# Optimization experiments

Measured on AMD Instinct MI355X. Metric: run time of the kernel, lower is better.

## Reference

```python
import jax, jax.numpy as jnp
import numpy as np

B, N, C, H = 8, 1024, 1024, 16
HD = C // H
SCALE = HD ** -0.5

def setup_inputs() -> dict:
    key = jax.random.key(0)
    k1, k2, k3, k4 = jax.random.split(key, 4)
    x = jax.random.normal(k1, (B, N, C), dtype=jnp.float32)
    # torch nn.Linear weights: [out, in]
    w_qkv = jax.random.normal(k2, (3 * C, C), dtype=jnp.float32) * (C ** -0.5)
    w_proj = jax.random.normal(k3, (C, C), dtype=jnp.float32) * (C ** -0.5)
    b_proj = jax.random.normal(k4, (C,), dtype=jnp.float32) * 0.02
    return {"x": x, "w_qkv": w_qkv, "w_proj": w_proj, "b_proj": b_proj}

def reference(x, w_qkv, w_proj, b_proj):
    Bv, Nv, Cv = x.shape
    # qkv projection (no bias); torch Linear: x @ W^T
    qkv = jnp.einsum('bnc,dc->bnd', x, w_qkv)
    qkv = qkv.reshape(Bv, Nv, 3, H, HD).transpose(2, 0, 3, 1, 4)  # [3,B,H,N,hd]
    q, k, v = qkv[0], qkv[1], qkv[2]
    attn = jnp.einsum('bhnd,bhmd->bhnm', q, k) * SCALE  # [B,H,N,N]
    attn = jax.nn.softmax(attn, axis=-1)
    out = jnp.einsum('bhnm,bhmd->bhnd', attn, v)
    out = out.transpose(0, 2, 1, 3).reshape(Bv, Nv, Cv)
    out = jnp.einsum('bnc,dc->bnd', out, w_proj) + b_proj
    return out
```

## Files before the change

kernel.cpp:

```cpp
#include <hip/hip_runtime.h>


typedef __attribute__((ext_vector_type(8))) short bf16x8;
typedef __attribute__((ext_vector_type(4))) short bf16x4;
typedef __attribute__((ext_vector_type(4))) float f32x4;

__device__ __forceinline__ short f2bf(float f) {
    union { float f; unsigned u; } x;
    x.f = f;
    unsigned r = x.u + 0x7fffu + ((x.u >> 16) & 1u);
    return (short)(r >> 16);
}

__device__ __forceinline__ void load_lds16(const void* g, void* l) {
    __builtin_amdgcn_global_load_lds((const __attribute__((address_space(1))) unsigned*)g,
                                     (__attribute__((address_space(3))) unsigned*)l,
                                     16, 0, 0);
}

__global__ __launch_bounds__(256) void convert_all(const float* __restrict__ x,
                                                   const float* __restrict__ wqkv,
                                                   const float* __restrict__ wproj,
                                                   short* __restrict__ xb,
                                                   short* __restrict__ wqkvb,
                                                   short* __restrict__ wprojb) {
    int i = blockIdx.x * 256 + threadIdx.x;
    const float* src;
    short* dst;
    int j;
    if (i < 2097152)      { src = x;     dst = xb;     j = i; }
    else if (i < 2883584) { src = wqkv;  dst = wqkvb;  j = i - 2097152; }
    else                  { src = wproj; dst = wprojb; j = i - 2883584; }
    float4 v = *(const float4*)(src + j * 4);
    unsigned lo = (unsigned short)f2bf(v.x) | ((unsigned)(unsigned short)f2bf(v.y) << 16);
    unsigned hi = (unsigned short)f2bf(v.z) | ((unsigned)(unsigned short)f2bf(v.w) << 16);
    uint2 p; p.x = lo; p.y = hi;
    *(uint2*)(dst + j * 4) = p;
}

template<int EPI, int BM, int BN, int NTX>
__global__ __launch_bounds__(512, 2) void gemm2p(const short* __restrict__ A,
                                                 const short* __restrict__ Bt,
                                                 short* __restrict__ q,
                                                 short* __restrict__ kk,
                                                 short* __restrict__ vt,
                                                 const float* __restrict__ bias,
                                                 float* __restrict__ out) {
    extern __shared__ short lds[];
    constexpr int AU = BM / 64, BU = BN / 64, NLD = AU + BU;
    constexpr int WM = BM / 2, WN = BN / 4;
    constexpr int MF = WM / 16, NF = WN / 16, MF2 = MF / 2;
    constexpr int NWG = (8192 / BM) * NTX;
    constexpr int CHUNK = NWG / 8;
    short* const As = lds;
    short* const Bs = lds + 2 * BM * 64;
    const int K = 1024;

    const int bid = blockIdx.x;
    const int tile = (bid & 7) * CHUNK + (bid >> 3);
    const int m0 = (tile / NTX) * BM;
    const int n0 = (tile % NTX) * BN;

    const int t = threadIdx.x;
    const int w = t >> 6, lane = t & 63, quad = lane >> 4, l16 = lane & 15;
    const int wm = (w >> 2) * WM, wn = (w & 3) * WN;
    const int sw = l16 & 7;

    const int srow = t >> 3;
    const int scol = ((t & 7) ^ (srow & 7)) * 8;
    const short* Ag = A  + (m0 + srow) * K + scol;
    const short* Bg = Bt + (n0 + srow) * K + scol;
    short* const Asw = As + (w * 8) * 64;
    short* const Bsw = Bs + (w * 8) * 64;

    f32x4 acc[MF][NF];
    #pragma unroll
    for (int mi = 0; mi < MF; ++mi)
        #pragma unroll
        for (int ni = 0; ni < NF; ++ni) acc[mi][ni] = (f32x4){0.f, 0.f, 0.f, 0.f};

    bf16x8 af[MF2][2], bf[NF][2];

#define STG_A(kt_, r_) load_lds16(Ag + (r_) * 64 * K + (kt_) * 64, Asw + ((kt_) & 1) * (BM * 64) + (r_) * 4096)
#define STG_B(kt_, r_) load_lds16(Bg + (r_) * 64 * K + (kt_) * 64, Bsw + ((kt_) & 1) * (BN * 64) + (r_) * 4096)
#define WAIT_VM_NLD() do { if constexpr (NLD == 7) asm volatile("s_waitcnt vmcnt(7)" ::: "memory"); \
                           else                    asm volatile("s_waitcnt vmcnt(6)" ::: "memory"); } while (0)

    #pragma unroll
    for (int r = 0; r < AU; ++r) STG_A(0, r);
    #pragma unroll
    for (int r = 0; r < BU; ++r) STG_B(0, r);
    #pragma unroll
    for (int r = 0; r < AU; ++r) STG_A(1, r);
    #pragma unroll
    for (int r = 0; r < BU; ++r) STG_B(1, r);
    WAIT_VM_NLD();
    asm volatile("s_barrier" ::: "memory");

    #pragma unroll
    for (int kt = 0; kt < 16; ++kt) {
        const short* Ar = As + (kt & 1) * (BM * 64);
        const short* Br = Bs + (kt & 1) * (BN * 64);

        #pragma unroll
        for (int mi = 0; mi < MF2; ++mi)
            #pragma unroll
            for (int c = 0; c < 2; ++c)
                af[mi][c] = *(const bf16x8*)(Ar + (wm + mi * 16 + l16) * 64 + (((quad + 4 * c) ^ sw) * 8));
        #pragma unroll
        for (int ni = 0; ni < NF; ++ni)
            #pragma unroll
            for (int c = 0; c < 2; ++c)
                bf[ni][c] = *(const bf16x8*)(Br + (wn + ni * 16 + l16) * 64 + (((quad + 4 * c) ^ sw) * 8));
        asm volatile("s_waitcnt lgkmcnt(0)" ::: "memory");
        __builtin_amdgcn_sched_barrier(0);
        __builtin_amdgcn_s_setprio(1);
        #pragma unroll
        for (int mi = 0; mi < MF2; ++mi)
            #pragma unroll
            for (int ni = 0; ni < NF; ++ni) {
                acc[mi][ni] = __builtin_amdgcn_mfma_f32_16x16x32_bf16(af[mi][0], bf[ni][0], acc[mi][ni], 0, 0, 0);
                acc[mi][ni] = __builtin_amdgcn_mfma_f32_16x16x32_bf16(af[mi][1], bf[ni][1], acc[mi][ni], 0, 0, 0);
            }
        __builtin_amdgcn_s_setprio(0);

        #pragma unroll
        for (int mi = 0; mi < MF2; ++mi)
            #pragma unroll
            for (int c = 0; c < 2; ++c)
                af[mi][c] = *(const bf16x8*)(Ar + (wm + (MF2 + mi) * 16 + l16) * 64 + (((quad + 4 * c) ^ sw) * 8));
        asm volatile("s_waitcnt lgkmcnt(0)" ::: "memory");
        __builtin_amdgcn_sched_barrier(0);
        __builtin_amdgcn_s_setprio(1);
        #pragma unroll
        for (int mi = 0; mi < MF2; ++mi)
            #pragma unroll
            for (int ni = 0; ni < NF; ++ni) {
                acc[MF2 + mi][ni] = __builtin_amdgcn_mfma_f32_16x16x32_bf16(af[mi][0], bf[ni][0], acc[MF2 + mi][ni], 0, 0, 0);
                acc[MF2 + mi][ni] = __builtin_amdgcn_mfma_f32_16x16x32_bf16(af[mi][1], bf[ni][1], acc[MF2 + mi][ni], 0, 0, 0);
            }
        __builtin_amdgcn_s_setprio(0);

        if (kt < 15) {
            asm volatile("s_barrier" ::: "memory");
            if (kt < 14) {
                #pragma unroll
                for (int r = 0; r < AU; ++r) STG_A(kt + 2, r);
                #pragma unroll
                for (int r = 0; r < BU; ++r) STG_B(kt + 2, r);
                WAIT_VM_NLD();
            } else {
                asm volatile("s_waitcnt vmcnt(0)" ::: "memory");
            }
            asm volatile("s_barrier" ::: "memory");
        }
    }
#undef STG_A
#undef STG_B
#undef WAIT_VM_NLD

    if (EPI == 0) {
        const float QS = 0.125f * 1.44269504088896f;
        #pragma unroll
        for (int ni = 0; ni < NF; ++ni) {
            int col = n0 + wn + ni * 16 + l16;
            int sect = col >> 10;
            int c = col & 1023;
            int h = c >> 6, dd = c & 63;
            #pragma unroll
            for (int mi = 0; mi < MF; ++mi) {
                #pragma unroll
                for (int r = 0; r < 4; ++r) {
                    int m = m0 + wm + mi * 16 + quad * 4 + r;
                    int b = m >> 10, i = m & 1023;
                    float v = acc[mi][ni][r];
                    if (sect == 0)      q[((b * 16 + h) * 1024 + i) * 64 + dd] = f2bf(v * QS);
                    else if (sect == 1) kk[((b * 16 + h) * 1024 + i) * 64 + dd] = f2bf(v);
                    else                vt[((b * 16 + h) * 64 + dd) * 1024 + i] = f2bf(v);
                }
            }
        }
    } else {
        #pragma unroll
        for (int ni = 0; ni < NF; ++ni) {
            int col = n0 + wn + ni * 16 + l16;
            float bv = bias[col];
            #pragma unroll
            for (int mi = 0; mi < MF; ++mi) {
                #pragma unroll
                for (int r = 0; r < 4; ++r) {
                    int m = m0 + wm + mi * 16 + quad * 4 + r;
                    out[m * 1024 + col] = acc[mi][ni][r] + bv;
                }
            }
        }
    }
}

__global__ __launch_bounds__(256) void attn_kernel(const short* __restrict__ q,
                                                   const short* __restrict__ k,
                                                   const short* __restrict__ vt,
                                                   short* __restrict__ ao) {
    __shared__ alignas(16) short Ks[2][64][72];
    __shared__ alignas(16) short Vs[2][64][72];

    const int bh = blockIdx.y, qt = blockIdx.x;
    const int t = threadIdx.x, w = t >> 6, lane = t & 63, quad = lane >> 4, l16 = lane & 15;
    const short* qg = q  + (bh * 1024 + qt * 128) * 64;
    const short* kg = k  + bh * 65536;
    const short* vg = vt + bh * 65536;

    bf16x8 qf[2][2];
    for (int mi = 0; mi < 2; ++mi) {
        const short* qr = qg + (w * 32 + mi * 16 + l16) * 64;
        qf[mi][0] = *(const bf16x8*)(qr + quad * 8);
        qf[mi][1] = *(const bf16x8*)(qr + 32 + quad * 8);
    }

    const int r0 = t >> 3,          c80 = (t & 7) * 8;
    const int r1 = (t + 256) >> 3,  c81 = c80;

    float rs[2] = {0.f, 0.f};
    f32x4 oaccT[2][4];
    for (int mi = 0; mi < 2; ++mi)
        for (int dt = 0; dt < 4; ++dt) oaccT[mi][dt] = (f32x4){0.f, 0.f, 0.f, 0.f};

    {
        float4 a = *(const float4*)&kg[r0 * 64 + c80];
        float4 b = *(const float4*)&kg[r1 * 64 + c81];
        float4 c = *(const float4*)&vg[r0 * 1024 + c80];
        float4 d = *(const float4*)&vg[r1 * 1024 + c81];
        *(float4*)&Ks[0][r0][c80] = a;  *(float4*)&Ks[0][r1][c81] = b;
        *(float4*)&Vs[0][r0][c80] = c;  *(float4*)&Vs[0][r1][c81] = d;
    }

    for (int jt = 0; jt < 16; ++jt) {
        const int cur = jt & 1;
        asm volatile("s_waitcnt lgkmcnt(0)" ::: "memory");
        asm volatile("s_barrier" ::: "memory");

        float4 kr0, kr1, vr0, vr1;
        if (jt < 15) {
            int jn = jt + 1;
            kr0 = *(const float4*)&kg[(jn * 64 + r0) * 64 + c80];
            kr1 = *(const float4*)&kg[(jn * 64 + r1) * 64 + c81];
            vr0 = *(const float4*)&vg[r0 * 1024 + jn * 64 + c80];
            vr1 = *(const float4*)&vg[r1 * 1024 + jn * 64 + c81];
        }

        for (int js = 0; js < 4; ++js) {
            bf16x8 kf0 = *(const bf16x8*)&Ks[cur][js * 16 + l16][quad * 8];
            bf16x8 kf1 = *(const bf16x8*)&Ks[cur][js * 16 + l16][32 + quad * 8];
            bf16x4 vtf[4];
            for (int dt = 0; dt < 4; ++dt)
                vtf[dt] = *(const bf16x4*)&Vs[cur][dt * 16 + l16][js * 16 + quad * 4];
            for (int mi = 0; mi < 2; ++mi) {
                f32x4 s = (f32x4){0.f, 0.f, 0.f, 0.f};
                s = __builtin_amdgcn_mfma_f32_16x16x32_bf16(kf0, qf[mi][0], s, 0, 0, 0);
                s = __builtin_amdgcn_mfma_f32_16x16x32_bf16(kf1, qf[mi][1], s, 0, 0, 0);
                bf16x4 pfrag;
                for (int r = 0; r < 4; ++r) {
                    float p = __builtin_amdgcn_exp2f(s[r]);
                    rs[mi] += p;
                    pfrag[r] = f2bf(p);
                }
                for (int dt = 0; dt < 4; ++dt)
                    oaccT[mi][dt] = __builtin_amdgcn_mfma_f32_16x16x16bf16_1k(
                        vtf[dt], pfrag, oaccT[mi][dt], 0, 0, 0);
            }
        }

        if (jt < 15) {
            const int nxt = cur ^ 1;
            *(float4*)&Ks[nxt][r0][c80] = kr0;  *(float4*)&Ks[nxt][r1][c81] = kr1;
            *(float4*)&Vs[nxt][r0][c80] = vr0;  *(float4*)&Vs[nxt][r1][c81] = vr1;
        }
    }

    for (int mi = 0; mi < 2; ++mi) {
        rs[mi] += __shfl_xor(rs[mi], 16, 64);
        rs[mi] += __shfl_xor(rs[mi], 32, 64);
    }

    const int b = bh >> 4, h = bh & 15;
    for (int mi = 0; mi < 2; ++mi) {
        float inv = 1.0f / rs[mi];
        int i = qt * 128 + w * 32 + mi * 16 + l16;
        short* aor = ao + (b * 1024 + i) * 1024 + h * 64;
        for (int dt = 0; dt < 4; ++dt) {
            bf16x4 o4;
            for (int r = 0; r < 4; ++r) o4[r] = f2bf(oaccT[mi][dt][r] * inv);
            *(bf16x4*)(aor + dt * 16 + quad * 4) = o4;
        }
    }
}

extern "C" void kernel_launch(void* const* d_in, const int* in_sizes, int n_in,
                              void* d_out, int out_size, void* d_ws, size_t ws_size,
                              hipStream_t stream) {
    const float* x      = (const float*)d_in[0];
    const float* w_qkv  = (const float*)d_in[1];
    const float* w_proj = (const float*)d_in[2];
    const float* b_proj = (const float*)d_in[3];
    float* out = (float*)d_out;

    char* ws = (char*)d_ws;
    short* xb     = (short*)(ws);
    short* wqkvb  = (short*)(ws + 16777216);
    short* wprojb = (short*)(ws + 23068672);
    short* qb     = (short*)(ws + 25165824);
    short* kb     = (short*)(ws + 41943040);
    short* vtb    = (short*)(ws + 58720256);
    short* aob    = (short*)(ws + 75497472);

    static bool s_init = false;
    if (!s_init) {
        hipFuncSetAttribute(reinterpret_cast<const void*>(&gemm2p<0, 256, 192, 16>),
                            hipFuncAttributeMaxDynamicSharedMemorySize, 114688);
        hipFuncSetAttribute(reinterpret_cast<const void*>(&gemm2p<1, 128, 256, 4>),
                            hipFuncAttributeMaxDynamicSharedMemorySize, 98304);
        s_init = true;
    }

    convert_all<<<12288, 256, 0, stream>>>(x, w_qkv, w_proj, xb, wqkvb, wprojb);
    gemm2p<0, 256, 192, 16><<<512, 512, 114688, stream>>>(xb, wqkvb, qb, kb, vtb, nullptr, nullptr);
    attn_kernel<<<dim3(8, 128), 256, 0, stream>>>(qb, kb, vtb, aob);
    gemm2p<1, 128, 256, 4><<<256, 512, 98304, stream>>>(aob, wprojb, nullptr, nullptr, nullptr, b_proj, out);
}
```

Baseline: 256.5 us.

## Restructure GEMM main loop into 8-phase schedule with interleaved global-to-LDS loads

Rewrites both projection GEMMs' k-loop into four compute phases per k-tile, each split by barriers. Global-to-LDS stage loads for the next tiles are spread across these phases instead of issued in one burst at the end of the iteration. The goal is to overlap memory traffic with MFMA work and keep loads in flight continuously. The cost is more barriers per iteration and a fragile hand-tuned load order, with vmcnt waits that must match what is still outstanding.

```diff
diff --git a/kernel.cpp b/kernel.cpp
--- a/kernel.cpp
+++ b/kernel.cpp
@@ -39,7 +39,7 @@
 }
 
 template<int EPI, int BM, int BN, int NTX>
-__global__ __launch_bounds__(512, 2) void gemm2p(const short* __restrict__ A,
+__global__ __launch_bounds__(512, 2) void gemm8p(const short* __restrict__ A,
                                                  const short* __restrict__ Bt,
                                                  short* __restrict__ q,
                                                  short* __restrict__ kk,
@@ -47,9 +47,8 @@
                                                  const float* __restrict__ bias,
                                                  float* __restrict__ out) {
     extern __shared__ short lds[];
-    constexpr int AU = BM / 64, BU = BN / 64, NLD = AU + BU;
     constexpr int WM = BM / 2, WN = BN / 4;
-    constexpr int MF = WM / 16, NF = WN / 16, MF2 = MF / 2;
+    constexpr int MF = WM / 16, NF = WN / 16, MH = MF / 2, HM = WM / 2;
     constexpr int NWG = (8192 / BM) * NTX;
     constexpr int CHUNK = NWG / 8;
     short* const As = lds;
@@ -70,8 +69,7 @@
     const int scol = ((t & 7) ^ (srow & 7)) * 8;
     const short* Ag = A  + (m0 + srow) * K + scol;
     const short* Bg = Bt + (n0 + srow) * K + scol;
-    short* const Asw = As + (w * 8) * 64;
-    short* const Bsw = Bs + (w * 8) * 64;
+    const int w8 = w * 8 * 64;
 
     f32x4 acc[MF][NF];
     #pragma unroll
@@ -79,85 +77,121 @@
         #pragma unroll
         for (int ni = 0; ni < NF; ++ni) acc[mi][ni] = (f32x4){0.f, 0.f, 0.f, 0.f};
 
-    bf16x8 af[MF2][2], bf[NF][2];
-
-#define STG_A(kt_, r_) load_lds16(Ag + (r_) * 64 * K + (kt_) * 64, Asw + ((kt_) & 1) * (BM * 64) + (r_) * 4096)
-#define STG_B(kt_, r_) load_lds16(Bg + (r_) * 64 * K + (kt_) * 64, Bsw + ((kt_) & 1) * (BN * 64) + (r_) * 4096)
-#define WAIT_VM_NLD() do { if constexpr (NLD == 7) asm volatile("s_waitcnt vmcnt(7)" ::: "memory"); \
-                           else                    asm volatile("s_waitcnt vmcnt(6)" ::: "memory"); } while (0)
-
-    #pragma unroll
-    for (int r = 0; r < AU; ++r) STG_A(0, r);
-    #pragma unroll
-    for (int r = 0; r < BU; ++r) STG_B(0, r);
-    #pragma unroll
-    for (int r = 0; r < AU; ++r) STG_A(1, r);
-    #pragma unroll
-    for (int r = 0; r < BU; ++r) STG_B(1, r);
-    WAIT_VM_NLD();
+    bf16x8 af[MH][2], bf[NF][2];
+
+#define STG_A(kt_, u_) load_lds16(Ag + (u_) * (64 * 1024) + (kt_) * 64, \
+                                  As + ((kt_) & 1) * (BM * 64) + (u_) * 4096 + w8)
+#define STG_B(kt_, u_) load_lds16(Bg + (u_) * (64 * 1024) + (kt_) * 64, \
+                                  Bs + ((kt_) & 1) * (BN * 64) + (u_) * 4096 + w8)
+
+    if (EPI == 0) {
+        STG_A(0, 0); STG_A(0, 1); STG_A(0, 2); STG_A(0, 3);
+        STG_B(0, 0); STG_B(0, 1); STG_B(0, 2);
+        STG_A(1, 0); STG_A(1, 2);
+    } else {
+        STG_B(0, 0); STG_B(0, 1); STG_B(0, 2); STG_B(0, 3);
+        STG_A(0, 0); STG_A(0, 1);
+        STG_A(1, 0); STG_A(1, 1);
+    }
+    asm volatile("s_waitcnt vmcnt(2)" ::: "memory");
     asm volatile("s_barrier" ::: "memory");
 
-    #pragma unroll
-    for (int kt = 0; kt < 16; ++kt) {
-        const short* Ar = As + (kt & 1) * (BM * 64);
-        const short* Br = Bs + (kt & 1) * (BN * 64);
-
-        #pragma unroll
-        for (int mi = 0; mi < MF2; ++mi)
+    auto ktbody = [&](int KT, bool ST1, bool ST2, bool LASTW) __attribute__((always_inline)) {
+        const short* Ar = As + (KT & 1) * (BM * 64);
+        const short* Br = Bs + (KT & 1) * (BN * 64);
+
+        #pragma unroll
+        for (int mi = 0; mi < MH; ++mi)
             #pragma unroll
             for (int c = 0; c < 2; ++c)
                 af[mi][c] = *(const bf16x8*)(Ar + (wm + mi * 16 + l16) * 64 + (((quad + 4 * c) ^ sw) * 8));
         #pragma unroll
-        for (int ni = 0; ni < NF; ++ni)
+        for (int ni = 0; ni < 2; ++ni)
             #pragma unroll
             for (int c = 0; c < 2; ++c)
                 bf[ni][c] = *(const bf16x8*)(Br + (wn + ni * 16 + l16) * 64 + (((quad + 4 * c) ^ sw) * 8));
+        if (EPI == 0) { if (ST1) { STG_A(KT + 1, 1); STG_A(KT + 1, 3); } }
+        else          { if (ST1) { STG_B(KT + 1, 0); STG_B(KT + 1, 1); } }
+        asm volatile("s_barrier" ::: "memory");
         asm volatile("s_waitcnt lgkmcnt(0)" ::: "memory");
         __builtin_amdgcn_sched_barrier(0);
         __builtin_amdgcn_s_setprio(1);
         #pragma unroll
-        for (int mi = 0; mi < MF2; ++mi)
-            #pragma unroll
-            for (int ni = 0; ni < NF; ++ni) {
+        for (int mi = 0; mi < MH; ++mi)
+            #pragma unroll
+            for (int ni = 0; ni < 2; ++ni) {
                 acc[mi][ni] = __builtin_amdgcn_mfma_f32_16x16x32_bf16(af[mi][0], bf[ni][0], acc[mi][ni], 0, 0, 0);
                 acc[mi][ni] = __builtin_amdgcn_mfma_f32_16x16x32_bf16(af[mi][1], bf[ni][1], acc[mi][ni], 0, 0, 0);
             }
         __builtin_amdgcn_s_setprio(0);
-
-        #pragma unroll
-        for (int mi = 0; mi < MF2; ++mi)
+        asm volatile("s_barrier" ::: "memory");
+
+        #pragma unroll
+        for (int ni = 2; ni < NF; ++ni)
             #pragma unroll
             for (int c = 0; c < 2; ++c)
-                af[mi][c] = *(const bf16x8*)(Ar + (wm + (MF2 + mi) * 16 + l16) * 64 + (((quad + 4 * c) ^ sw) * 8));
+                bf[ni][c] = *(const bf16x8*)(Br + (wn + ni * 16 + l16) * 64 + (((quad + 4 * c) ^ sw) * 8));
+        if (EPI == 0) { if (ST1) { STG_B(KT + 1, 0); STG_B(KT + 1, 1); STG_B(KT + 1, 2); } }
+        else          { if (ST1) { STG_B(KT + 1, 2); STG_B(KT + 1, 3); } }
+        asm volatile("s_barrier" ::: "memory");
         asm volatile("s_waitcnt lgkmcnt(0)" ::: "memory");
         __builtin_amdgcn_sched_barrier(0);
         __builtin_amdgcn_s_setprio(1);
         #pragma unroll
-        for (int mi = 0; mi < MF2; ++mi)
-            #pragma unroll
-            for (int ni = 0; ni < NF; ++ni) {
-                acc[MF2 + mi][ni] = __builtin_amdgcn_mfma_f32_16x16x32_bf16(af[mi][0], bf[ni][0], acc[MF2 + mi][ni], 0, 0, 0);
-                acc[MF2 + mi][ni] = __builtin_amdgcn_mfma_f32_16x16x32_bf16(af[mi][1], bf[ni][1], acc[MF2 + mi][ni], 0, 0, 0);
+        for (int mi = 0; mi < MH; ++mi)
+            #pragma unroll
+            for (int ni = 2; ni < NF; ++ni) {
+                acc[mi][ni] = __builtin_amdgcn_mfma_f32_16x16x32_bf16(af[mi][0], bf[ni][0], acc[mi][ni], 0, 0, 0);
+                acc[mi][ni] = __builtin_amdgcn_mfma_f32_16x16x32_bf16(af[mi][1], bf[ni][1], acc[mi][ni], 0, 0, 0);
             }
         __builtin_amdgcn_s_setprio(0);
-
-        if (kt < 15) {
-            asm volatile("s_barrier" ::: "memory");
-            if (kt < 14) {
-                #pragma unroll
-                for (int r = 0; r < AU; ++r) STG_A(kt + 2, r);
-                #pragma unroll
-                for (int r = 0; r < BU; ++r) STG_B(kt + 2, r);
-                WAIT_VM_NLD();
-            } else {
-                asm volatile("s_waitcnt vmcnt(0)" ::: "memory");
-            }
-            asm volatile("s_barrier" ::: "memory");
-        }
+        asm volatile("s_barrier" ::: "memory");
+
+        #pragma unroll
+        for (int mi = 0; mi < MH; ++mi)
+            #pragma unroll
+            for (int c = 0; c < 2; ++c)
+                af[mi][c] = *(const bf16x8*)(Ar + (wm + HM + mi * 16 + l16) * 64 + (((quad + 4 * c) ^ sw) * 8));
+        if (EPI == 0) { if (ST2) { STG_A(KT + 2, 0); STG_A(KT + 2, 2); } }
+        asm volatile("s_barrier" ::: "memory");
+        asm volatile("s_waitcnt lgkmcnt(0)" ::: "memory");
+        __builtin_amdgcn_sched_barrier(0);
+        __builtin_amdgcn_s_setprio(1);
+        #pragma unroll
+        for (int mi = 0; mi < MH; ++mi)
+            #pragma unroll
+            for (int ni = 0; ni < 2; ++ni) {
+                acc[MH + mi][ni] = __builtin_amdgcn_mfma_f32_16x16x32_bf16(af[mi][0], bf[ni][0], acc[MH + mi][ni], 0, 0, 0);
+                acc[MH + mi][ni] = __builtin_amdgcn_mfma_f32_16x16x32_bf16(af[mi][1], bf[ni][1], acc[MH + mi][ni], 0, 0, 0);
+            }
+        __builtin_amdgcn_s_setprio(0);
+        asm volatile("s_barrier" ::: "memory");
+
+        if (EPI == 1) { if (ST2) { STG_A(KT + 2, 0); STG_A(KT + 2, 1); } }
+        asm volatile("s_barrier" ::: "memory");
+        asm volatile("s_waitcnt lgkmcnt(0)" ::: "memory");
+        __builtin_amdgcn_sched_barrier(0);
+        __builtin_amdgcn_s_setprio(1);
+        #pragma unroll
+        for (int mi = 0; mi < MH; ++mi)
+            #pragma unroll
+            for (int ni = 2; ni < NF; ++ni) {
+                acc[MH + mi][ni] = __builtin_amdgcn_mfma_f32_16x16x32_bf16(af[mi][0], bf[ni][0], acc[MH + mi][ni], 0, 0, 0);
+                acc[MH + mi][ni] = __builtin_amdgcn_mfma_f32_16x16x32_bf16(af[mi][1], bf[ni][1], acc[MH + mi][ni], 0, 0, 0);
+            }
+        __builtin_amdgcn_s_setprio(0);
+        if (LASTW) asm volatile("s_waitcnt vmcnt(0)" ::: "memory");
+        else       asm volatile("s_waitcnt vmcnt(2)" ::: "memory");
+        asm volatile("s_barrier" ::: "memory");
+    };
+
+    #pragma unroll 1
+    for (int j = 0; j < 8; ++j) {
+        ktbody(2 * j,     true,  j < 7, j == 7);
+        ktbody(2 * j + 1, j < 7, j < 7, false);
     }
 #undef STG_A
 #undef STG_B
-#undef WAIT_VM_NLD
 
     if (EPI == 0) {
         const float QS = 0.125f * 1.44269504088896f;
@@ -315,15 +349,15 @@
 
     static bool s_init = false;
     if (!s_init) {
-        hipFuncSetAttribute(reinterpret_cast<const void*>(&gemm2p<0, 256, 192, 16>),
+        hipFuncSetAttribute(reinterpret_cast<const void*>(&gemm8p<0, 256, 192, 16>),
                             hipFuncAttributeMaxDynamicSharedMemorySize, 114688);
-        hipFuncSetAttribute(reinterpret_cast<const void*>(&gemm2p<1, 128, 256, 4>),
+        hipFuncSetAttribute(reinterpret_cast<const void*>(&gemm8p<1, 128, 256, 4>),
                             hipFuncAttributeMaxDynamicSharedMemorySize, 98304);
         s_init = true;
     }
 
     convert_all<<<12288, 256, 0, stream>>>(x, w_qkv, w_proj, xb, wqkvb, wprojb);
-    gemm2p<0, 256, 192, 16><<<512, 512, 114688, stream>>>(xb, wqkvb, qb, kb, vtb, nullptr, nullptr);
+    gemm8p<0, 256, 192, 16><<<512, 512, 114688, stream>>>(xb, wqkvb, qb, kb, vtb, nullptr, nullptr);
     attn_kernel<<<dim3(8, 128), 256, 0, stream>>>(qb, kb, vtb, aob);
-    gemm2p<1, 128, 256, 4><<<256, 512, 98304, stream>>>(aob, wprojb, nullptr, nullptr, nullptr, b_proj, out);
-}
+    gemm8p<1, 128, 256, 4><<<256, 512, 98304, stream>>>(aob, wprojb, nullptr, nullptr, nullptr, b_proj, out);
+}
```

After: 256.2 us. No clear change (-0.1%).

## Replace double-buffered large-tile GEMM with simple single-buffered 128x128 GEMM

Applied to the files above, without the earlier changes.

Swaps the double-buffered, large-tile (256x192 / 128x256, 512-thread) GEMM for a simpler 128x128-tile, 256-thread kernel that uses single-buffered static LDS and a __syncthreads before and after each K-step load. This gives smaller tiles, more workgroups and higher occupancy (3 blocks per CU) while dropping the prefetch pipeline and the manual scheduling hints. It risks exposing global-load latency and reducing data reuse per tile.

```diff
diff --git a/kernel.cpp b/kernel.cpp
--- a/kernel.cpp
+++ b/kernel.cpp
@@ -38,137 +38,84 @@
     *(uint2*)(dst + j * 4) = p;
 }
 
-template<int EPI, int BM, int BN, int NTX>
-__global__ __launch_bounds__(512, 2) void gemm2p(const short* __restrict__ A,
+template<int EPI, int NTX>
+__global__ __launch_bounds__(256, 3) void gemm97(const short* __restrict__ A,
                                                  const short* __restrict__ Bt,
                                                  short* __restrict__ q,
                                                  short* __restrict__ kk,
                                                  short* __restrict__ vt,
                                                  const float* __restrict__ bias,
                                                  float* __restrict__ out) {
-    extern __shared__ short lds[];
-    constexpr int AU = BM / 64, BU = BN / 64, NLD = AU + BU;
-    constexpr int WM = BM / 2, WN = BN / 4;
-    constexpr int MF = WM / 16, NF = WN / 16, MF2 = MF / 2;
-    constexpr int NWG = (8192 / BM) * NTX;
+    __shared__ alignas(16) short As[128][64];
+    __shared__ alignas(16) short Bs[128][64];
+    const int K = 1024;
+    constexpr int NWG = 64 * NTX;
     constexpr int CHUNK = NWG / 8;
-    short* const As = lds;
-    short* const Bs = lds + 2 * BM * 64;
-    const int K = 1024;
 
     const int bid = blockIdx.x;
     const int tile = (bid & 7) * CHUNK + (bid >> 3);
-    const int m0 = (tile / NTX) * BM;
-    const int n0 = (tile % NTX) * BN;
+    const int m0 = (tile / NTX) * 128;
+    const int n0 = (tile % NTX) * 128;
 
     const int t = threadIdx.x;
     const int w = t >> 6, lane = t & 63, quad = lane >> 4, l16 = lane & 15;
-    const int wm = (w >> 2) * WM, wn = (w & 3) * WN;
+    const int wm = (w >> 1) * 64, wn = (w & 1) * 64;
     const int sw = l16 & 7;
 
     const int srow = t >> 3;
     const int scol = ((t & 7) ^ (srow & 7)) * 8;
     const short* Ag = A  + (m0 + srow) * K + scol;
     const short* Bg = Bt + (n0 + srow) * K + scol;
-    short* const Asw = As + (w * 8) * 64;
-    short* const Bsw = Bs + (w * 8) * 64;
-
-    f32x4 acc[MF][NF];
+    short* const Asw = &As[w * 8][0];
+    short* const Bsw = &Bs[w * 8][0];
+
+    f32x4 acc[4][4];
     #pragma unroll
-    for (int mi = 0; mi < MF; ++mi)
-        #pragma unroll
-        for (int ni = 0; ni < NF; ++ni) acc[mi][ni] = (f32x4){0.f, 0.f, 0.f, 0.f};
-
-    bf16x8 af[MF2][2], bf[NF][2];
-
-#define STG_A(kt_, r_) load_lds16(Ag + (r_) * 64 * K + (kt_) * 64, Asw + ((kt_) & 1) * (BM * 64) + (r_) * 4096)
-#define STG_B(kt_, r_) load_lds16(Bg + (r_) * 64 * K + (kt_) * 64, Bsw + ((kt_) & 1) * (BN * 64) + (r_) * 4096)
-#define WAIT_VM_NLD() do { if constexpr (NLD == 7) asm volatile("s_waitcnt vmcnt(7)" ::: "memory"); \
-                           else                    asm volatile("s_waitcnt vmcnt(6)" ::: "memory"); } while (0)
-
-    #pragma unroll
-    for (int r = 0; r < AU; ++r) STG_A(0, r);
-    #pragma unroll
-    for (int r = 0; r < BU; ++r) STG_B(0, r);
-    #pragma unroll
-    for (int r = 0; r < AU; ++r) STG_A(1, r);
-    #pragma unroll
-    for (int r = 0; r < BU; ++r) STG_B(1, r);
-    WAIT_VM_NLD();
-    asm volatile("s_barrier" ::: "memory");
-
-    #pragma unroll
+    for (int mi = 0; mi < 4; ++mi)
+        #pragma unroll
+        for (int ni = 0; ni < 4; ++ni) acc[mi][ni] = (f32x4){0.f, 0.f, 0.f, 0.f};
+
+    #pragma unroll 1
     for (int kt = 0; kt < 16; ++kt) {
-        const short* Ar = As + (kt & 1) * (BM * 64);
-        const short* Br = Bs + (kt & 1) * (BN * 64);
-
-        #pragma unroll
-        for (int mi = 0; mi < MF2; ++mi)
+        __syncthreads();
+        #pragma unroll
+        for (int r = 0; r < 4; ++r)
+            load_lds16(Ag + r * 32 * K + kt * 64, Asw + r * 32 * 64);
+        #pragma unroll
+        for (int r = 0; r < 4; ++r)
+            load_lds16(Bg + r * 32 * K + kt * 64, Bsw + r * 32 * 64);
+        __syncthreads();
+
+        bf16x8 af[4][2], bf[4][2];
+        #pragma unroll
+        for (int mi = 0; mi < 4; ++mi)
             #pragma unroll
             for (int c = 0; c < 2; ++c)
-                af[mi][c] = *(const bf16x8*)(Ar + (wm + mi * 16 + l16) * 64 + (((quad + 4 * c) ^ sw) * 8));
-        #pragma unroll
-        for (int ni = 0; ni < NF; ++ni)
+                af[mi][c] = *(const bf16x8*)&As[wm + mi * 16 + l16][((quad + 4 * c) ^ sw) * 8];
+        #pragma unroll
+        for (int ni = 0; ni < 4; ++ni)
             #pragma unroll
             for (int c = 0; c < 2; ++c)
-                bf[ni][c] = *(const bf16x8*)(Br + (wn + ni * 16 + l16) * 64 + (((quad + 4 * c) ^ sw) * 8));
-        asm volatile("s_waitcnt lgkmcnt(0)" ::: "memory");
-        __builtin_amdgcn_sched_barrier(0);
-        __builtin_amdgcn_s_setprio(1);
-        #pragma unroll
-        for (int mi = 0; mi < MF2; ++mi)
-            #pragma unroll
-            for (int ni = 0; ni < NF; ++ni) {
+                bf[ni][c] = *(const bf16x8*)&Bs[wn + ni * 16 + l16][((quad + 4 * c) ^ sw) * 8];
+        #pragma unroll
+        for (int mi = 0; mi < 4; ++mi)
+            #pragma unroll
+            for (int ni = 0; ni < 4; ++ni) {
                 acc[mi][ni] = __builtin_amdgcn_mfma_f32_16x16x32_bf16(af[mi][0], bf[ni][0], acc[mi][ni], 0, 0, 0);
                 acc[mi][ni] = __builtin_amdgcn_mfma_f32_16x16x32_bf16(af[mi][1], bf[ni][1], acc[mi][ni], 0, 0, 0);
             }
-        __builtin_amdgcn_s_setprio(0);
-
-        #pragma unroll
-        for (int mi = 0; mi < MF2; ++mi)
-            #pragma unroll
-            for (int c = 0; c < 2; ++c)
-                af[mi][c] = *(const bf16x8*)(Ar + (wm + (MF2 + mi) * 16 + l16) * 64 + (((quad + 4 * c) ^ sw) * 8));
-        asm volatile("s_waitcnt lgkmcnt(0)" ::: "memory");
-        __builtin_amdgcn_sched_barrier(0);
-        __builtin_amdgcn_s_setprio(1);
-        #pragma unroll
-        for (int mi = 0; mi < MF2; ++mi)
-            #pragma unroll
-            for (int ni = 0; ni < NF; ++ni) {
-                acc[MF2 + mi][ni] = __builtin_amdgcn_mfma_f32_16x16x32_bf16(af[mi][0], bf[ni][0], acc[MF2 + mi][ni], 0, 0, 0);
-                acc[MF2 + mi][ni] = __builtin_amdgcn_mfma_f32_16x16x32_bf16(af[mi][1], bf[ni][1], acc[MF2 + mi][ni], 0, 0, 0);
-            }
-        __builtin_amdgcn_s_setprio(0);
-
-        if (kt < 15) {
-            asm volatile("s_barrier" ::: "memory");
-            if (kt < 14) {
-                #pragma unroll
-                for (int r = 0; r < AU; ++r) STG_A(kt + 2, r);
-                #pragma unroll
-                for (int r = 0; r < BU; ++r) STG_B(kt + 2, r);
-                WAIT_VM_NLD();
-            } else {
-                asm volatile("s_waitcnt vmcnt(0)" ::: "memory");
-            }
-            asm volatile("s_barrier" ::: "memory");
-        }
-    }
-#undef STG_A
-#undef STG_B
-#undef WAIT_VM_NLD
+    }
 
     if (EPI == 0) {
         const float QS = 0.125f * 1.44269504088896f;
         #pragma unroll
-        for (int ni = 0; ni < NF; ++ni) {
+        for (int ni = 0; ni < 4; ++ni) {
             int col = n0 + wn + ni * 16 + l16;
             int sect = col >> 10;
             int c = col & 1023;
             int h = c >> 6, dd = c & 63;
             #pragma unroll
-            for (int mi = 0; mi < MF; ++mi) {
+            for (int mi = 0; mi < 4; ++mi) {
                 #pragma unroll
                 for (int r = 0; r < 4; ++r) {
                     int m = m0 + wm + mi * 16 + quad * 4 + r;
@@ -182,11 +129,11 @@
         }
     } else {
         #pragma unroll
-        for (int ni = 0; ni < NF; ++ni) {
+        for (int ni = 0; ni < 4; ++ni) {
             int col = n0 + wn + ni * 16 + l16;
             float bv = bias[col];
             #pragma unroll
-            for (int mi = 0; mi < MF; ++mi) {
+            for (int mi = 0; mi < 4; ++mi) {
                 #pragma unroll
                 for (int r = 0; r < 4; ++r) {
                     int m = m0 + wm + mi * 16 + quad * 4 + r;
@@ -313,17 +260,8 @@
     short* vtb    = (short*)(ws + 58720256);
     short* aob    = (short*)(ws + 75497472);
 
-    static bool s_init = false;
-    if (!s_init) {
-        hipFuncSetAttribute(reinterpret_cast<const void*>(&gemm2p<0, 256, 192, 16>),
-                            hipFuncAttributeMaxDynamicSharedMemorySize, 114688);
-        hipFuncSetAttribute(reinterpret_cast<const void*>(&gemm2p<1, 128, 256, 4>),
-                            hipFuncAttributeMaxDynamicSharedMemorySize, 98304);
-        s_init = true;
-    }
-
     convert_all<<<12288, 256, 0, stream>>>(x, w_qkv, w_proj, xb, wqkvb, wprojb);
-    gemm2p<0, 256, 192, 16><<<512, 512, 114688, stream>>>(xb, wqkvb, qb, kb, vtb, nullptr, nullptr);
+    gemm97<0, 24><<<1536, 256, 0, stream>>>(xb, wqkvb, qb, kb, vtb, nullptr, nullptr);
     attn_kernel<<<dim3(8, 128), 256, 0, stream>>>(qb, kb, vtb, aob);
-    gemm2p<1, 128, 256, 4><<<256, 512, 98304, stream>>>(aob, wprojb, nullptr, nullptr, nullptr, b_proj, out);
-}
+    gemm97<1, 8><<<512, 256, 0, stream>>>(aob, wprojb, nullptr, nullptr, nullptr, b_proj, out);
+}
```

New measurement: 240.0 us. -6.5%, faster.
